# Kernel optimization log

Measured on AMD Instinct MI355X. Metric: run time of the kernel, lower is better.

Reference implementation:

```python
import jax, jax.numpy as jnp
import numpy as np

D_IN = 1024
D_OUT = 1024
NUM_HEADS = 16
HEAD_DIM = D_OUT // NUM_HEADS


def setup_inputs() -> dict:
    key = jax.random.key(0)
    ks = jax.random.split(key, 6)
    s = 1.0 / np.sqrt(D_IN)
    inputs = jax.random.normal(ks[0], (4, 2048, D_IN), dtype=jnp.float32)
    Wq = jax.random.uniform(ks[1], (D_IN, D_OUT), jnp.float32, -s, s)
    Wk = jax.random.uniform(ks[2], (D_IN, D_OUT), jnp.float32, -s, s)
    Wv = jax.random.uniform(ks[3], (D_IN, D_OUT), jnp.float32, -s, s)
    so = 1.0 / np.sqrt(D_OUT)
    Wo = jax.random.uniform(ks[4], (D_OUT, D_OUT), jnp.float32, -so, so)
    bo = jax.random.uniform(ks[5], (D_OUT,), jnp.float32, -so, so)
    return {"inputs": inputs, "Wq": Wq, "Wk": Wk, "Wv": Wv, "Wo": Wo, "bo": bo}


def reference(inputs, Wq, Wk, Wv, Wo, bo):
    b, n, _ = inputs.shape
    # projections -> [b, h, n, d]
    def split_heads(x):
        return x.reshape(b, n, NUM_HEADS, HEAD_DIM).transpose(0, 2, 1, 3)
    q = split_heads(inputs @ Wq)
    k = split_heads(inputs @ Wk)
    v = split_heads(inputs @ Wv)
    scores = jnp.einsum('bhqd,bhkd->bhqk', q, k) / np.sqrt(HEAD_DIM).astype(np.float32)
    causal = jnp.tril(jnp.ones((n, n), dtype=bool))  # True = keep
    scores = jnp.where(causal, scores, -jnp.inf)
    weights = jax.nn.softmax(scores, axis=-1)
    ctx = jnp.einsum('bhqk,bhkd->bhqd', weights, v)
    ctx = ctx.transpose(0, 2, 1, 3).reshape(b, n, D_OUT)
    return ctx @ Wo + bo
```

## Files before the change

kernel.cpp:

```cpp
#include <hip/hip_runtime.h>

typedef unsigned short u16;
typedef unsigned int u32;
typedef __attribute__((ext_vector_type(8))) short short8;
typedef __attribute__((ext_vector_type(4))) short short4_t;
typedef __attribute__((ext_vector_type(4))) float floatx4;
typedef __attribute__((ext_vector_type(4))) unsigned short ushort4_t;
typedef __attribute__((ext_vector_type(4))) float float4_t;
typedef __attribute__((ext_vector_type(2))) unsigned int uint2_t;


__device__ __forceinline__ u16 f2bf(float f) {
  unsigned u = __builtin_bit_cast(unsigned, f);
  u += 0x7FFFu + ((u >> 16) & 1u);
  return (u16)(u >> 16);
}

__device__ __forceinline__ u32 pack_bf2(float a, float b) {
  u32 ua = __builtin_bit_cast(u32, a) + 0x8000u;
  u32 ub = __builtin_bit_cast(u32, b) + 0x8000u;
  return __builtin_amdgcn_perm(ua, ub, 0x07060302u);
}

__device__ __forceinline__ void gload_lds16(const void* g, void* l) {
  __builtin_amdgcn_global_load_lds(
      (const __attribute__((address_space(1))) void*)g,
      (__attribute__((address_space(3))) void*)l, 16, 0, 0);
}


__global__ void cvt_x(const float* __restrict__ src, u16* __restrict__ dst) {
  int i = blockIdx.x * 256 + threadIdx.x;
  float4_t f = ((const float4_t*)src)[i];
  ushort4_t u;
  u.x = f2bf(f.x); u.y = f2bf(f.y); u.z = f2bf(f.z); u.w = f2bf(f.w);
  ((ushort4_t*)dst)[i] = u;
}

__global__ __launch_bounds__(256) void transpose_cvt4(
    const float* __restrict__ wq, const float* __restrict__ wk,
    const float* __restrict__ wv, const float* __restrict__ wo,
    u16* __restrict__ qk, u16* __restrict__ vt, u16* __restrict__ ot, float sc) {
  __shared__ float T[64][65];
  const int which = blockIdx.z;
  const float* s = (which == 0) ? wq : (which == 1) ? wk : (which == 2) ? wv : wo;
  u16* d = (which == 0) ? qk : (which == 1) ? (qk + (1u << 20)) : (which == 2) ? vt : ot;
  const float scale = (which == 0) ? sc : 1.f;
  const int n0 = blockIdx.x * 64, k0 = blockIdx.y * 64;
  const int c = threadIdx.x & 63, rg = threadIdx.x >> 6;
  for (int i = 0; i < 16; ++i) {
    int r = i * 4 + rg;
    T[r][c] = s[(k0 + r) * 1024 + n0 + c];
  }
  __syncthreads();
  for (int i = 0; i < 16; ++i) {
    int r = i * 4 + rg;
    d[(n0 + r) * 1024 + k0 + c] = f2bf(T[c][r] * scale);
  }
}

template <int MODE>
__global__ __launch_bounds__(256) void gemm_bt(
    const u16* __restrict__ A, const u16* __restrict__ Bt, void* __restrict__ Cv,
    const float* __restrict__ bias, int K, int lda, int ldb, int ldc) {
  __shared__ u16 As[2][128 * 32];
  __shared__ u16 Bs[2][128 * 32];
  const int tid = threadIdx.x;
  const int w = tid >> 6, l = tid & 63, quad = l >> 4, l16 = l & 15;
  const int wm = w >> 1, wn = w & 1;
  const size_t m0 = (size_t)blockIdx.y * 128, n0 = (size_t)blockIdx.x * 128;

  floatx4 acc[4][4];
  for (int i = 0; i < 4; ++i)
    for (int j = 0; j < 4; ++j) acc[i][j] = (floatx4){0.f, 0.f, 0.f, 0.f};

  auto stage = [&](int k0, int buf) {
    for (int i = 0; i < 2; ++i) {
      int c = i * 256 + tid;
      int row = c >> 2, off = (c & 3) * 8;
      gload_lds16(A + (m0 + row) * (size_t)lda + k0 + off, &As[buf][c * 8]);
      gload_lds16(Bt + (n0 + row) * (size_t)ldb + k0 + off, &Bs[buf][c * 8]);
    }
  };

  const int nk = K >> 5;
  stage(0, 0);
  __syncthreads();

  for (int ki = 0; ki < nk; ++ki) {
    const int buf = ki & 1;
    if (ki + 1 < nk) stage((ki + 1) << 5, buf ^ 1);

    short8 a[4], bb[4];
    for (int im = 0; im < 4; ++im)
      a[im] = *(const short8*)&As[buf][(wm * 64 + im * 16 + l16) * 32 + quad * 8];
    for (int in = 0; in < 4; ++in)
      bb[in] = *(const short8*)&Bs[buf][(wn * 64 + in * 16 + l16) * 32 + quad * 8];
    for (int im = 0; im < 4; ++im)
      for (int in = 0; in < 4; ++in)
        acc[im][in] = __builtin_amdgcn_mfma_f32_16x16x32_bf16(a[im], bb[in], acc[im][in], 0, 0, 0);

    __syncthreads();
  }

  for (int im = 0; im < 4; ++im)
    for (int in = 0; in < 4; ++in) {
      size_t r0 = m0 + wm * 64 + im * 16 + quad * 4;
      size_t col = n0 + wn * 64 + in * 16 + l16;
      float bv = (MODE == 1) ? bias[col] : 0.f;
      for (int r = 0; r < 4; ++r) {
        float val = acc[im][in][r] + bv;
        if (MODE == 0)
          ((u16*)Cv)[(r0 + r) * (size_t)ldc + col] = f2bf(val);
        else
          ((float*)Cv)[(r0 + r) * (size_t)ldc + col] = val;
      }
    }
}

__global__ __launch_bounds__(256, 2) void flash_attn(
    const u16* __restrict__ QK, const u16* __restrict__ Vt, u16* __restrict__ ctx) {
  __shared__ u16 Ks[2][64 * 64];
  __shared__ u16 Vs[2][64 * 64];

  const int tid = threadIdx.x;
  const int w = tid >> 6, l = tid & 63, quad = l >> 4, l16 = l & 15;
  const int bh = blockIdx.x, p = blockIdx.y;
  const int b = bh >> 4, h = bh & 15;
  const int xr = (l16 & 7) << 4;

  const int qtA = 15 - p, qtB = p;
  const int nktA = 2 * qtA + 2, ntot = nktA + 2 * qtB + 2;

  auto stage = [&](int kt, int buf) {
    for (int i = 0; i < 2; ++i) {
      int c = i * 256 + tid;
      int row = c >> 3, scol = ((c & 7) ^ (row & 7)) << 3;
      gload_lds16(QK + (size_t)(b * 2048 + kt * 64 + row) * 2048 + 1024 + h * 64 + scol,
                  &Ks[buf][c * 8]);
      gload_lds16(Vt + (size_t)(h * 64 + row) * 8192 + b * 2048 + kt * 64 + scol,
                  &Vs[buf][c * 8]);
    }
  };

  short8 aq[2][2];
  floatx4 o[2][4];
  float lsum[2];

  auto load_q = [&](int q0w) {
    for (int qf = 0; qf < 2; ++qf) {
      const size_t base = (size_t)(b * 2048 + q0w + qf * 16 + l16) * 2048 + h * 64 + quad * 8;
      aq[qf][0] = *(const short8*)(QK + base);
      aq[qf][1] = *(const short8*)(QK + base + 32);
    }
    for (int qf = 0; qf < 2; ++qf) {
      lsum[qf] = 0.f;
      for (int df = 0; df < 4; ++df) o[qf][df] = (floatx4){0.f, 0.f, 0.f, 0.f};
    }
  };

  auto epilogue = [&](int q0w) {
    for (int qf = 0; qf < 2; ++qf) {
      float t = lsum[qf];
      t += __shfl_xor(t, 16, 64);
      t += __shfl_xor(t, 32, 64);
      float inv = __builtin_amdgcn_rcpf(t);
      size_t row = (size_t)(b * 2048 + q0w + qf * 16 + l16);
      for (int df = 0; df < 4; ++df) {
        ushort4_t st;
        for (int r = 0; r < 4; ++r) st[r] = f2bf(o[qf][df][r] * inv);
        *(ushort4_t*)(ctx + row * 1024 + h * 64 + df * 16 + quad * 4) = st;
      }
    }
  };

  int q0w = qtA * 128 + w * 32;
  int ktmax_w = (q0w + 31) >> 6;
  load_q(q0w);
  stage(0, 0);
  __syncthreads();

  for (int t = 0; t < ntot; ++t) {
    const int buf = t & 1;
    const int kt = (t < nktA) ? t : t - nktA;
    if (t + 1 < ntot) {
      int tn = t + 1;
      stage((tn < nktA) ? tn : tn - nktA, buf ^ 1);
    }

    if (kt <= ktmax_w) {
      const bool need_mask = (kt == ktmax_w);

      short8 ka[4][2];
      for (int nf = 0; nf < 4; ++nf) {
        const char* kb = (const char*)&Ks[buf][0] + (nf * 16 + l16) * 128;
        ka[nf][0] = *(const short8*)(kb + ((quad * 16) ^ xr));
        ka[nf][1] = *(const short8*)(kb + ((64 + quad * 16) ^ xr));
      }
      short4_t va[4][4];
      for (int df = 0; df < 4; ++df) {
        const char* vb = (const char*)&Vs[buf][0] + (df * 16 + l16) * 128;
        for (int nf = 0; nf < 4; ++nf)
          va[nf][df] = *(const short4_t*)(vb + ((nf * 32 + quad * 8) ^ xr));
      }

      for (int qf = 0; qf < 2; ++qf) {
        floatx4 s[4];
        for (int nf = 0; nf < 4; ++nf) s[nf] = (floatx4){0.f, 0.f, 0.f, 0.f};
        for (int nf = 0; nf < 4; ++nf) {
          s[nf] = __builtin_amdgcn_mfma_f32_16x16x32_bf16(ka[nf][0], aq[qf][0], s[nf], 0, 0, 0);
          s[nf] = __builtin_amdgcn_mfma_f32_16x16x32_bf16(ka[nf][1], aq[qf][1], s[nf], 0, 0, 0);
        }
        if (need_mask) {
          int qpos = q0w + qf * 16 + l16;
          for (int nf = 0; nf < 4; ++nf)
            for (int r = 0; r < 4; ++r) {
              int kpos = kt * 64 + nf * 16 + quad * 4 + r;
              if (kpos > qpos) s[nf][r] = -1e30f;
            }
        }
        for (int nf = 0; nf < 4; ++nf) {
          float p0 = __builtin_amdgcn_exp2f(s[nf][0]);
          float p1 = __builtin_amdgcn_exp2f(s[nf][1]);
          float p2 = __builtin_amdgcn_exp2f(s[nf][2]);
          float p3 = __builtin_amdgcn_exp2f(s[nf][3]);
          lsum[qf] += (p0 + p1) + (p2 + p3);
          uint2_t pk;
          pk.x = pack_bf2(p1, p0);
          pk.y = pack_bf2(p3, p2);
          short4_t pb = __builtin_bit_cast(short4_t, pk);
          for (int df = 0; df < 4; ++df)
            o[qf][df] = __builtin_amdgcn_mfma_f32_16x16x16bf16_1k(va[nf][df], pb, o[qf][df], 0, 0, 0);
        }
      }
    }
    __syncthreads();

    if (t == nktA - 1) {
      epilogue(q0w);
      q0w = qtB * 128 + w * 32;
      ktmax_w = (q0w + 31) >> 6;
      load_q(q0w);
    }
  }
  epilogue(q0w);
}


extern "C" void kernel_launch(void* const* d_in, const int* in_sizes, int n_in,
                              void* d_out, int out_size, void* d_ws, size_t ws_size,
                              hipStream_t stream) {
  const float* X  = (const float*)d_in[0];
  const float* Wq = (const float*)d_in[1];
  const float* Wk = (const float*)d_in[2];
  const float* Wv = (const float*)d_in[3];
  const float* Wo = (const float*)d_in[4];
  const float* bo = (const float*)d_in[5];

  char* ws = (char*)d_ws;
  u16* Xb   = (u16*)(ws);
  u16* WqkT = (u16*)(ws + (16u << 20));
  u16* WvT  = (u16*)(ws + (20u << 20));
  u16* WoT  = (u16*)(ws + (22u << 20));
  u16* QKb  = (u16*)(ws + (24u << 20));
  u16* Vt   = (u16*)(ws + (56u << 20));

  const float SC = 0.125f * 1.44269504088896340736f;

  cvt_x<<<8192, 256, 0, stream>>>(X, Xb);
  transpose_cvt4<<<dim3(16, 16, 4), 256, 0, stream>>>(Wq, Wk, Wv, Wo, WqkT, WvT, WoT, SC);

  gemm_bt<0><<<dim3(16, 64), 256, 0, stream>>>(Xb, WqkT, QKb, nullptr, 1024, 1024, 1024, 2048);
  gemm_bt<0><<<dim3(64, 8), 256, 0, stream>>>(WvT, Xb, Vt, nullptr, 1024, 1024, 1024, 8192);

  flash_attn<<<dim3(64, 8), 256, 0, stream>>>(QKb, Vt, Xb);

  gemm_bt<1><<<dim3(8, 64), 256, 0, stream>>>(Xb, WoT, (float*)d_out, bo, 1024, 1024, 1024, 1024);
}
```

Measured before the change: 261.5 us.

## Use 8 waves per attention block with 16 query rows per wave

The flash attention kernel moves from 256 to 512 threads per block. Each wave now handles 16 query rows instead of 32, and each thread stages one chunk of K/V into LDS instead of two. This cuts per-wave register use and adds waves so more latency can be hidden. In exchange, each K/V fragment read from LDS feeds half as many MFMAs, so LDS read traffic per unit of work roughly doubles, and with more waves per block the per-tile __syncthreads barriers synchronize more waves.

```diff
diff --git a/kernel.cpp b/kernel.cpp
--- a/kernel.cpp
+++ b/kernel.cpp
@@ -118,7 +118,7 @@
     }
 }
 
-__global__ __launch_bounds__(256, 2) void flash_attn(
+__global__ __launch_bounds__(512, 4) void flash_attn(
     const u16* __restrict__ QK, const u16* __restrict__ Vt, u16* __restrict__ ctx) {
   __shared__ u16 Ks[2][64 * 64];
   __shared__ u16 Vs[2][64 * 64];
@@ -133,50 +133,43 @@
   const int nktA = 2 * qtA + 2, ntot = nktA + 2 * qtB + 2;
 
   auto stage = [&](int kt, int buf) {
-    for (int i = 0; i < 2; ++i) {
-      int c = i * 256 + tid;
-      int row = c >> 3, scol = ((c & 7) ^ (row & 7)) << 3;
-      gload_lds16(QK + (size_t)(b * 2048 + kt * 64 + row) * 2048 + 1024 + h * 64 + scol,
-                  &Ks[buf][c * 8]);
-      gload_lds16(Vt + (size_t)(h * 64 + row) * 8192 + b * 2048 + kt * 64 + scol,
-                  &Vs[buf][c * 8]);
-    }
-  };
-
-  short8 aq[2][2];
-  floatx4 o[2][4];
-  float lsum[2];
-
-  auto load_q = [&](int q0w) {
-    for (int qf = 0; qf < 2; ++qf) {
-      const size_t base = (size_t)(b * 2048 + q0w + qf * 16 + l16) * 2048 + h * 64 + quad * 8;
-      aq[qf][0] = *(const short8*)(QK + base);
-      aq[qf][1] = *(const short8*)(QK + base + 32);
-    }
-    for (int qf = 0; qf < 2; ++qf) {
-      lsum[qf] = 0.f;
-      for (int df = 0; df < 4; ++df) o[qf][df] = (floatx4){0.f, 0.f, 0.f, 0.f};
-    }
-  };
-
-  auto epilogue = [&](int q0w) {
-    for (int qf = 0; qf < 2; ++qf) {
-      float t = lsum[qf];
-      t += __shfl_xor(t, 16, 64);
-      t += __shfl_xor(t, 32, 64);
-      float inv = __builtin_amdgcn_rcpf(t);
-      size_t row = (size_t)(b * 2048 + q0w + qf * 16 + l16);
-      for (int df = 0; df < 4; ++df) {
-        ushort4_t st;
-        for (int r = 0; r < 4; ++r) st[r] = f2bf(o[qf][df][r] * inv);
-        *(ushort4_t*)(ctx + row * 1024 + h * 64 + df * 16 + quad * 4) = st;
-      }
-    }
-  };
-
-  int q0w = qtA * 128 + w * 32;
-  int ktmax_w = (q0w + 31) >> 6;
-  load_q(q0w);
+    int c = tid;
+    int row = c >> 3, scol = ((c & 7) ^ (row & 7)) << 3;
+    gload_lds16(QK + (size_t)(b * 2048 + kt * 64 + row) * 2048 + 1024 + h * 64 + scol,
+                &Ks[buf][c * 8]);
+    gload_lds16(Vt + (size_t)(h * 64 + row) * 8192 + b * 2048 + kt * 64 + scol,
+                &Vs[buf][c * 8]);
+  };
+
+  short8 aq[2];
+  floatx4 o[4];
+  float lsum;
+  int q0w, ktmax_w;
+
+  auto load_q = [&](int qt) {
+    q0w = qt * 128 + w * 16;
+    ktmax_w = (q0w + 15) >> 6;
+    const size_t base = (size_t)(b * 2048 + q0w + l16) * 2048 + h * 64 + quad * 8;
+    aq[0] = *(const short8*)(QK + base);
+    aq[1] = *(const short8*)(QK + base + 32);
+    lsum = 0.f;
+    for (int df = 0; df < 4; ++df) o[df] = (floatx4){0.f, 0.f, 0.f, 0.f};
+  };
+
+  auto epilogue = [&]() {
+    float t = lsum;
+    t += __shfl_xor(t, 16, 64);
+    t += __shfl_xor(t, 32, 64);
+    float inv = __builtin_amdgcn_rcpf(t);
+    size_t row = (size_t)(b * 2048 + q0w + l16);
+    for (int df = 0; df < 4; ++df) {
+      ushort4_t st;
+      for (int r = 0; r < 4; ++r) st[r] = f2bf(o[df][r] * inv);
+      *(ushort4_t*)(ctx + row * 1024 + h * 64 + df * 16 + quad * 4) = st;
+    }
+  };
+
+  load_q(qtA);
   stage(0, 0);
   __syncthreads();
 
@@ -204,46 +197,42 @@
           va[nf][df] = *(const short4_t*)(vb + ((nf * 32 + quad * 8) ^ xr));
       }
 
-      for (int qf = 0; qf < 2; ++qf) {
-        floatx4 s[4];
-        for (int nf = 0; nf < 4; ++nf) s[nf] = (floatx4){0.f, 0.f, 0.f, 0.f};
-        for (int nf = 0; nf < 4; ++nf) {
-          s[nf] = __builtin_amdgcn_mfma_f32_16x16x32_bf16(ka[nf][0], aq[qf][0], s[nf], 0, 0, 0);
-          s[nf] = __builtin_amdgcn_mfma_f32_16x16x32_bf16(ka[nf][1], aq[qf][1], s[nf], 0, 0, 0);
-        }
-        if (need_mask) {
-          int qpos = q0w + qf * 16 + l16;
-          for (int nf = 0; nf < 4; ++nf)
-            for (int r = 0; r < 4; ++r) {
-              int kpos = kt * 64 + nf * 16 + quad * 4 + r;
-              if (kpos > qpos) s[nf][r] = -1e30f;
-            }
-        }
-        for (int nf = 0; nf < 4; ++nf) {
-          float p0 = __builtin_amdgcn_exp2f(s[nf][0]);
-          float p1 = __builtin_amdgcn_exp2f(s[nf][1]);
-          float p2 = __builtin_amdgcn_exp2f(s[nf][2]);
-          float p3 = __builtin_amdgcn_exp2f(s[nf][3]);
-          lsum[qf] += (p0 + p1) + (p2 + p3);
-          uint2_t pk;
-          pk.x = pack_bf2(p1, p0);
-          pk.y = pack_bf2(p3, p2);
-          short4_t pb = __builtin_bit_cast(short4_t, pk);
-          for (int df = 0; df < 4; ++df)
-            o[qf][df] = __builtin_amdgcn_mfma_f32_16x16x16bf16_1k(va[nf][df], pb, o[qf][df], 0, 0, 0);
-        }
+      floatx4 s[4];
+      for (int nf = 0; nf < 4; ++nf) s[nf] = (floatx4){0.f, 0.f, 0.f, 0.f};
+      for (int nf = 0; nf < 4; ++nf) {
+        s[nf] = __builtin_amdgcn_mfma_f32_16x16x32_bf16(ka[nf][0], aq[0], s[nf], 0, 0, 0);
+        s[nf] = __builtin_amdgcn_mfma_f32_16x16x32_bf16(ka[nf][1], aq[1], s[nf], 0, 0, 0);
+      }
+      if (need_mask) {
+        int qpos = q0w + l16;
+        for (int nf = 0; nf < 4; ++nf)
+          for (int r = 0; r < 4; ++r) {
+            int kpos = kt * 64 + nf * 16 + quad * 4 + r;
+            if (kpos > qpos) s[nf][r] = -1e30f;
+          }
+      }
+      for (int nf = 0; nf < 4; ++nf) {
+        float p0 = __builtin_amdgcn_exp2f(s[nf][0]);
+        float p1 = __builtin_amdgcn_exp2f(s[nf][1]);
+        float p2 = __builtin_amdgcn_exp2f(s[nf][2]);
+        float p3 = __builtin_amdgcn_exp2f(s[nf][3]);
+        lsum += (p0 + p1) + (p2 + p3);
+        uint2_t pk;
+        pk.x = pack_bf2(p1, p0);
+        pk.y = pack_bf2(p3, p2);
+        short4_t pb = __builtin_bit_cast(short4_t, pk);
+        for (int df = 0; df < 4; ++df)
+          o[df] = __builtin_amdgcn_mfma_f32_16x16x16bf16_1k(va[nf][df], pb, o[df], 0, 0, 0);
       }
     }
     __syncthreads();
 
     if (t == nktA - 1) {
-      epilogue(q0w);
-      q0w = qtB * 128 + w * 32;
-      ktmax_w = (q0w + 31) >> 6;
-      load_q(q0w);
-    }
-  }
-  epilogue(q0w);
+      epilogue();
+      load_q(qtB);
+    }
+  }
+  epilogue();
 }
 
 
@@ -273,7 +262,7 @@
   gemm_bt<0><<<dim3(16, 64), 256, 0, stream>>>(Xb, WqkT, QKb, nullptr, 1024, 1024, 1024, 2048);
   gemm_bt<0><<<dim3(64, 8), 256, 0, stream>>>(WvT, Xb, Vt, nullptr, 1024, 1024, 1024, 8192);
 
-  flash_attn<<<dim3(64, 8), 256, 0, stream>>>(QKb, Vt, Xb);
+  flash_attn<<<dim3(64, 8), 512, 0, stream>>>(QKb, Vt, Xb);
 
   gemm_bt<1><<<dim3(8, 64), 256, 0, stream>>>(Xb, WoT, (float*)d_out, bo, 1024, 1024, 1024, 1024);
 }
```

Result: no change. 262.6 us (+0.4%).

## Split KV tiles across two wave groups in flash attention and combine via LDS

Applied to the files above, without the earlier changes.

Doubles the flash attention block to 512 threads, with wave groups taking alternating (even/odd) key tiles for the same query rows. Partial outputs and row sums are merged through a new shared-memory buffer before normalization and store. The aim is more waves in flight to hide latency within the same 512-block grid, and each thread now issues a single staging load. The cost is extra LDS, added barriers for the combine, and higher register pressure from the 512,4 launch bounds.

```diff
diff --git a/kernel.cpp b/kernel.cpp
--- a/kernel.cpp
+++ b/kernel.cpp
@@ -118,13 +118,15 @@
     }
 }
 
-__global__ __launch_bounds__(256, 2) void flash_attn(
+__global__ __launch_bounds__(512, 4) void flash_attn(
     const u16* __restrict__ QK, const u16* __restrict__ Vt, u16* __restrict__ ctx) {
   __shared__ u16 Ks[2][64 * 64];
   __shared__ u16 Vs[2][64 * 64];
+  __shared__ float Comb[4][64][18];
 
   const int tid = threadIdx.x;
   const int w = tid >> 6, l = tid & 63, quad = l >> 4, l16 = l & 15;
+  const int qg = w & 3, kp = w >> 2;
   const int bh = blockIdx.x, p = blockIdx.y;
   const int b = bh >> 4, h = bh & 15;
   const int xr = (l16 & 7) << 4;
@@ -133,50 +135,65 @@
   const int nktA = 2 * qtA + 2, ntot = nktA + 2 * qtB + 2;
 
   auto stage = [&](int kt, int buf) {
-    for (int i = 0; i < 2; ++i) {
-      int c = i * 256 + tid;
-      int row = c >> 3, scol = ((c & 7) ^ (row & 7)) << 3;
-      gload_lds16(QK + (size_t)(b * 2048 + kt * 64 + row) * 2048 + 1024 + h * 64 + scol,
-                  &Ks[buf][c * 8]);
-      gload_lds16(Vt + (size_t)(h * 64 + row) * 8192 + b * 2048 + kt * 64 + scol,
-                  &Vs[buf][c * 8]);
-    }
+    int c = tid;
+    int row = c >> 3, scol = ((c & 7) ^ (row & 7)) << 3;
+    gload_lds16(QK + (size_t)(b * 2048 + kt * 64 + row) * 2048 + 1024 + h * 64 + scol,
+                &Ks[buf][c * 8]);
+    gload_lds16(Vt + (size_t)(h * 64 + row) * 8192 + b * 2048 + kt * 64 + scol,
+                &Vs[buf][c * 8]);
   };
 
   short8 aq[2][2];
   floatx4 o[2][4];
   float lsum[2];
-
-  auto load_q = [&](int q0w) {
+  int q0w, ktmax_w;
+
+  auto load_q = [&](int qt) {
+    q0w = qt * 128 + qg * 32;
+    ktmax_w = (q0w + 31) >> 6;
     for (int qf = 0; qf < 2; ++qf) {
       const size_t base = (size_t)(b * 2048 + q0w + qf * 16 + l16) * 2048 + h * 64 + quad * 8;
       aq[qf][0] = *(const short8*)(QK + base);
       aq[qf][1] = *(const short8*)(QK + base + 32);
-    }
-    for (int qf = 0; qf < 2; ++qf) {
       lsum[qf] = 0.f;
       for (int df = 0; df < 4; ++df) o[qf][df] = (floatx4){0.f, 0.f, 0.f, 0.f};
     }
   };
 
-  auto epilogue = [&](int q0w) {
+  auto combine_epilogue = [&]() {
     for (int qf = 0; qf < 2; ++qf) {
-      float t = lsum[qf];
-      t += __shfl_xor(t, 16, 64);
-      t += __shfl_xor(t, 32, 64);
-      float inv = __builtin_amdgcn_rcpf(t);
-      size_t row = (size_t)(b * 2048 + q0w + qf * 16 + l16);
-      for (int df = 0; df < 4; ++df) {
-        ushort4_t st;
-        for (int r = 0; r < 4; ++r) st[r] = f2bf(o[qf][df][r] * inv);
-        *(ushort4_t*)(ctx + row * 1024 + h * 64 + df * 16 + quad * 4) = st;
-      }
-    }
-  };
-
-  int q0w = qtA * 128 + w * 32;
-  int ktmax_w = (q0w + 31) >> 6;
-  load_q(q0w);
+      if (kp == 1) {
+        float* dst = &Comb[qg][l][0];
+        for (int df = 0; df < 4; ++df)
+          for (int r = 0; r < 4; ++r) dst[df * 4 + r] = o[qf][df][r];
+        dst[16] = lsum[qf];
+      }
+      __syncthreads();
+      if (kp == 0) {
+        const float* src = &Comb[qg][l][0];
+        for (int df = 0; df < 4; ++df)
+          for (int r = 0; r < 4; ++r) o[qf][df][r] += src[df * 4 + r];
+        lsum[qf] += src[16];
+      }
+      __syncthreads();
+    }
+    if (kp == 0) {
+      for (int qf = 0; qf < 2; ++qf) {
+        float t = lsum[qf];
+        t += __shfl_xor(t, 16, 64);
+        t += __shfl_xor(t, 32, 64);
+        float inv = __builtin_amdgcn_rcpf(t);
+        size_t row = (size_t)(b * 2048 + q0w + qf * 16 + l16);
+        for (int df = 0; df < 4; ++df) {
+          ushort4_t st;
+          for (int r = 0; r < 4; ++r) st[r] = f2bf(o[qf][df][r] * inv);
+          *(ushort4_t*)(ctx + row * 1024 + h * 64 + df * 16 + quad * 4) = st;
+        }
+      }
+    }
+  };
+
+  load_q(qtA);
   stage(0, 0);
   __syncthreads();
 
@@ -188,7 +205,7 @@
       stage((tn < nktA) ? tn : tn - nktA, buf ^ 1);
     }
 
-    if (kt <= ktmax_w) {
+    if (kt <= ktmax_w && (kt & 1) == kp) {
       const bool need_mask = (kt == ktmax_w);
 
       short8 ka[4][2];
@@ -237,13 +254,11 @@
     __syncthreads();
 
     if (t == nktA - 1) {
-      epilogue(q0w);
-      q0w = qtB * 128 + w * 32;
-      ktmax_w = (q0w + 31) >> 6;
-      load_q(q0w);
-    }
-  }
-  epilogue(q0w);
+      combine_epilogue();
+      load_q(qtB);
+    }
+  }
+  combine_epilogue();
 }
 
 
@@ -273,7 +288,7 @@
   gemm_bt<0><<<dim3(16, 64), 256, 0, stream>>>(Xb, WqkT, QKb, nullptr, 1024, 1024, 1024, 2048);
   gemm_bt<0><<<dim3(64, 8), 256, 0, stream>>>(WvT, Xb, Vt, nullptr, 1024, 1024, 1024, 8192);
 
-  flash_attn<<<dim3(64, 8), 256, 0, stream>>>(QKb, Vt, Xb);
+  flash_attn<<<dim3(64, 8), 512, 0, stream>>>(QKb, Vt, Xb);
 
   gemm_bt<1><<<dim3(8, 64), 256, 0, stream>>>(Xb, WoT, (float*)d_out, bo, 1024, 1024, 1024, 1024);
 }
```

Measured after the change: 469.4 us. +79.5%, slower.
